# Kernel tuning notes

Hardware: AMD Instinct MI355X
Metric: run time of the kernel (lower is better)

Reference implementation:

```python
import jax, jax.numpy as jnp
import numpy as np

N_NODES = 50000
N_FEATURES = 128
HIDDEN = 64
N_EDGES = 1600000


def gcn_conv(x, src, dst, edge_w, W, b, num_nodes):
    """torch_geometric GCNConv with edge weights: add self-loops (weight 1),
    symmetric deg^-1/2 normalization, aggregate into dst, then bias."""
    loop = jnp.arange(num_nodes)
    src_f = jnp.concatenate([src, loop])
    dst_f = jnp.concatenate([dst, loop])
    w_f = jnp.concatenate([edge_w, jnp.ones((num_nodes,), dtype=edge_w.dtype)])
    deg = jax.ops.segment_sum(w_f, dst_f, num_segments=num_nodes)
    dinv = jnp.where(deg > 0, jax.lax.rsqrt(deg), 0.0)
    norm = dinv[src_f] * w_f * dinv[dst_f]            # [E+N]
    h = x @ W                                          # [N, out]
    msg = h[src_f] * norm[:, None]                     # [E+N, out]
    out = jax.ops.segment_sum(msg, dst_f, num_segments=num_nodes)
    return out + b


def setup_inputs() -> dict:
    key = jax.random.key(0)
    ks = jax.random.split(key, 12)
    features = jax.random.normal(ks[0], (N_NODES, N_FEATURES), dtype=jnp.float32)
    edge_index = jax.random.randint(ks[1], (2, N_EDGES), 0, N_NODES, dtype=jnp.int64)
    edge_attr = jax.random.uniform(ks[2], (N_EDGES,), dtype=jnp.float32)
    s = 0.05
    W1 = jax.random.normal(ks[3], (N_FEATURES, HIDDEN), dtype=jnp.float32) * s
    b1 = jnp.zeros((HIDDEN,), dtype=jnp.float32)
    W2 = jax.random.normal(ks[4], (HIDDEN, HIDDEN // 2), dtype=jnp.float32) * s
    b2 = jnp.zeros((HIDDEN // 2,), dtype=jnp.float32)
    Wd = jax.random.normal(ks[5], (N_FEATURES, 2), dtype=jnp.float32) * s
    bd = jnp.zeros((2,), dtype=jnp.float32)
    w_fc = jax.random.normal(ks[6], (N_NODES * 2,), dtype=jnp.float32) * s
    b_fc = jnp.zeros((), dtype=jnp.float32)
    return {"features": features, "edge_index": edge_index, "edge_attr": edge_attr,
            "W1": W1, "b1": b1, "W2": W2, "b2": b2, "Wd": Wd, "bd": bd,
            "w_fc": w_fc, "b_fc": b_fc}


def reference(features, edge_index, edge_attr, W1, b1, W2, b2, Wd, bd, w_fc, b_fc):
    N = features.shape[0]
    src, dst = edge_index[0], edge_index[1]
    # --- generator encoder (GAE.encode): GCN -> relu -> GCN -> tanh ---
    h = gcn_conv(features, src, dst, edge_attr, W1, b1, N)
    h = jax.nn.relu(h)                                  # dropout inactive (eval)
    z = jnp.tanh(gcn_conv(h, src, dst, edge_attr, W2, b2, N))  # [N, HIDDEN//2]
    # --- residual path: tile z to n_features width and add input features ---
    rep = features.shape[1] // z.shape[1]
    x = jnp.tile(z, (1, rep)) + features                # [N, n_features]
    # (edge_probabilities = z@z.T + rebuilt adjacency is computed by the
    #  generator but discarded by GraphCounteRGAN.forward -> dead code)
    # --- discriminator: GCN -> relu -> flatten -> fc -> sigmoid ---
    d = jax.nn.relu(gcn_conv(x, src, dst, edge_attr, Wd, bd, N))  # [N, 2]
    logit = jnp.dot(d.reshape(-1), w_fc) + b_fc
    return jax.nn.sigmoid(logit)
```

## Files before the change

kernel.cpp:

```cpp
#include <hip/hip_runtime.h>
#include <math.h>

#define BLK 256
#define CHUNK 4096
#define BSH 8
#define BNODES 256
#define MAXNB 256

typedef __attribute__((ext_vector_type(8))) short bf8_t;
typedef __attribute__((ext_vector_type(4))) float f4_t;

__device__ __forceinline__ unsigned short f2bf(float f) {
    unsigned u = __float_as_uint(f);
    u += 0x7FFFu + ((u >> 16) & 1u);
    return (unsigned short)(u >> 16);
}
__device__ __forceinline__ float bf2f(unsigned short b) {
    return __uint_as_float(((unsigned)b) << 16);
}

__global__ void detect_kernel(const int* __restrict__ idx, int E,
                              int* __restrict__ flag, float* __restrict__ acc,
                              int* __restrict__ done) {
    int t = threadIdx.x;
    long long j = (long long)t * (E / 64);
    int hi = idx[2 * j + 1];
    unsigned long long b = __ballot(hi != 0);
    if (t == 0) { *flag = (b == 0ULL) ? 1 : 0; *acc = 0.f; *done = 0; }
}

__global__ __launch_bounds__(256) void bucket_hist_kernel(const int* __restrict__ idx,
                                                          int* __restrict__ blockCnt,
                                                          int E, int NB) {
    __shared__ int hist[MAXNB];
    __shared__ int i64s;
    int t = threadIdx.x;
    for (int i = t; i < NB; i += 256) hist[i] = 0;
    if (t < 64) {
        long long j = (long long)t * (E / 64);
        int hi = idx[2 * j + 1];
        unsigned long long b = __ballot(hi != 0);
        if (t == 0) i64s = (b == 0ULL) ? 1 : 0;
    }
    __syncthreads();
    bool i64 = i64s != 0;
    int e0 = blockIdx.x * CHUNK;
    int e1 = min(e0 + CHUNK, E);
    for (int e = e0 + t; e < e1; e += 256) {
        int d = i64 ? idx[2 * (E + e)] : idx[E + e];
        atomicAdd(&hist[d >> BSH], 1);
    }
    __syncthreads();
    for (int i = t; i < NB; i += 256) blockCnt[blockIdx.x * NB + i] = hist[i];
}

__global__ __launch_bounds__(256) void col_scan_kernel(const int* __restrict__ blockCnt,
                                                       int* __restrict__ blockBase,
                                                       int* __restrict__ bucketTotal,
                                                       int NBLK, int NB,
                                                       float* __restrict__ acc,
                                                       int* __restrict__ done) {
    __shared__ int s[256];
    __shared__ int carry;
    int bkt = blockIdx.x;
    int t = threadIdx.x;
    if (bkt == 0 && t == 0) { *acc = 0.f; *done = 0; }
    if (t == 0) carry = 0;
    __syncthreads();
    for (int base = 0; base < NBLK; base += 256) {
        int i = base + t;
        int v = (i < NBLK) ? blockCnt[i * NB + bkt] : 0;
        s[t] = v;
        __syncthreads();
        for (int off = 1; off < 256; off <<= 1) {
            int x = (t >= off) ? s[t - off] : 0;
            __syncthreads();
            s[t] += x;
            __syncthreads();
        }
        if (i < NBLK) blockBase[i * NB + bkt] = carry + s[t] - v;
        __syncthreads();
        if (t == 0) carry += s[255];
        __syncthreads();
    }
    if (t == 0) bucketTotal[bkt] = carry;
}

__global__ __launch_bounds__(256) void bucket_scatter_kernel(const int* __restrict__ idx,
                                                             const float* __restrict__ ew,
                                                             const int* __restrict__ bucketTotal,
                                                             const int* __restrict__ blockBase,
                                                             int2* __restrict__ temp,
                                                             int E, int NB) {
    __shared__ int base[MAXNB];
    __shared__ int fill[MAXNB];
    __shared__ int s[256];
    __shared__ int i64s;
    int t = threadIdx.x;
    int v = (t < NB) ? bucketTotal[t] : 0;
    s[t] = v;
    if (t < 64) {
        long long j = (long long)t * (E / 64);
        int hi = idx[2 * j + 1];
        unsigned long long b = __ballot(hi != 0);
        if (t == 0) i64s = (b == 0ULL) ? 1 : 0;
    }
    __syncthreads();
    for (int off = 1; off < 256; off <<= 1) {
        int x = (t >= off) ? s[t - off] : 0;
        __syncthreads();
        s[t] += x;
        __syncthreads();
    }
    if (t < NB) {
        base[t] = (s[t] - v) + blockBase[blockIdx.x * NB + t];
        fill[t] = 0;
    }
    __syncthreads();
    bool i64 = i64s != 0;
    int e0 = blockIdx.x * CHUNK;
    int e1 = min(e0 + CHUNK, E);
    for (int e = e0 + t; e < e1; e += 256) {
        int s_, d;
        if (i64) { s_ = idx[2 * e]; d = idx[2 * (E + e)]; }
        else     { s_ = idx[e];     d = idx[E + e]; }
        float w = ew[e];
        int b = d >> BSH;
        int pos = base[b] + atomicAdd(&fill[b], 1);
        temp[pos] = make_int2(s_ | ((d & (BNODES - 1)) << 16), __float_as_int(w));
    }
}

__global__ __launch_bounds__(512) void csr_build_kernel(const int2* __restrict__ temp,
                                                        const int* __restrict__ bucketTotal,
                                                        unsigned* __restrict__ csrw,
                                                        int* __restrict__ row,
                                                        float* __restrict__ dinv,
                                                        int N, int NB, int E) {
    __shared__ int cnt[BNODES];
    __shared__ float dw[BNODES];
    __shared__ int offs[BNODES];
    __shared__ int sb[256];
    int bkt = blockIdx.x;
    int t = threadIdx.x;
    int node0 = bkt << BSH;
    int nn = min(BNODES, N - node0);
    if (t < BNODES) { cnt[t] = 0; dw[t] = 0.f; }
    if (t < 256) sb[t] = (t < NB) ? bucketTotal[t] : 0;
    __syncthreads();
    for (int off = 1; off < 256; off <<= 1) {
        int x = 0;
        if (t < 256 && t >= off) x = sb[t - off];
        __syncthreads();
        if (t < 256) sb[t] += x;
        __syncthreads();
    }
    int p0 = (bkt > 0) ? sb[bkt - 1] : 0;
    int p1 = sb[bkt];
    for (int p = p0 + t; p < p1; p += 512) {
        int2 v = temp[p];
        int dl = (v.x >> 16) & (BNODES - 1);
        atomicAdd(&cnt[dl], 1);
        atomicAdd(&dw[dl], __int_as_float(v.y));
    }
    __syncthreads();
    int v = 0;
    if (t < BNODES) { v = cnt[t]; offs[t] = v; }
    __syncthreads();
    for (int off = 1; off < BNODES; off <<= 1) {
        int x = 0;
        if (t < BNODES && t >= off) x = offs[t - off];
        __syncthreads();
        if (t < BNODES) offs[t] += x;
        __syncthreads();
    }
    if (t < BNODES) {
        int excl = offs[t] - v;
        if (t < nn) {
            row[node0 + t] = p0 + excl;
            dinv[node0 + t] = rsqrtf(1.f + dw[t]);
        }
        offs[t] = excl;
    }
    if (bkt == NB - 1 && t == 0) row[N] = E;
    __syncthreads();
    if (t < BNODES) cnt[t] = 0;
    __syncthreads();
    for (int p = p0 + t; p < p1; p += 512) {
        int2 v2 = temp[p];
        int dl = (v2.x >> 16) & (BNODES - 1);
        int pos = p0 + offs[dl] + atomicAdd(&cnt[dl], 1);
        unsigned wb = (unsigned)v2.y;
        wb += 0x7FFFu + ((wb >> 16) & 1u);
        csrw[pos] = ((unsigned)v2.x & 0xFFFFu) | (wb & 0xFFFF0000u);
    }
}

__global__ __launch_bounds__(256) void gather64_kernel(const int* __restrict__ row,
                                                       const unsigned* __restrict__ csrw,
                                                       const unsigned short* __restrict__ h,
                                                       const float* __restrict__ dinv,
                                                       const float* __restrict__ bias,
                                                       float* __restrict__ out, int N) {
    int wid = (blockIdx.x * 256 + threadIdx.x) >> 6;
    int o = threadIdx.x & 63;
    if (wid >= N) return;
    float di = dinv[wid];
    int p0 = row[wid], p1 = row[wid + 1];
    const unsigned short* hb = h + o;
    float es[4] = {0.f, 0.f, 0.f, 0.f};
    for (int p = p0; p < p1; p += 64) {
        int q = p + o;
        unsigned pe = (q < p1) ? csrw[q] : 0u;
        int m = min(64, p1 - p);
        int mp = (m + 15) & ~15;
        for (int j = 0; j < mp; j += 16) {
            unsigned ee[16];
            float hh[16];
#pragma unroll
            for (int u = 0; u < 16; ++u) ee[u] = (unsigned)__shfl((int)pe, j + u, 64);
#pragma unroll
            for (int u = 0; u < 16; ++u) hh[u] = bf2f(hb[(ee[u] & 0xFFFFu) * 64]);
#pragma unroll
            for (int u = 0; u < 16; ++u)
                es[u & 3] = fmaf(__uint_as_float(ee[u] & 0xFFFF0000u), hh[u], es[u & 3]);
        }
    }
    float e01 = es[0] + es[1], e23 = es[2] + es[3];
    out[wid * 64 + o] = bias[o] + di * (bf2f(h[(size_t)wid * 64 + o]) + e01 + e23);
}

__global__ __launch_bounds__(256) void gather32_kernel(const int* __restrict__ row,
                                                       const unsigned* __restrict__ csrw,
                                                       const unsigned short* __restrict__ h,
                                                       const float* __restrict__ dinv,
                                                       const float* __restrict__ bias,
                                                       float* __restrict__ out, int N) {
    int wid = (blockIdx.x * 256 + threadIdx.x) >> 6;
    int lane = threadIdx.x & 63;
    int o = lane & 31;
    int g = lane >> 5;
    if (wid >= N) return;
    float di = dinv[wid];
    int p0 = row[wid], p1 = row[wid + 1];
    const unsigned short* hb = h + o;
    float es[4] = {0.f, 0.f, 0.f, 0.f};
    for (int p = p0; p < p1; p += 64) {
        int q = p + lane;
        unsigned pe = (q < p1) ? csrw[q] : 0u;
        int m = min(64, p1 - p);
        int mp = (m + 15) & ~15;
        for (int j = g; j < mp; j += 16) {
            unsigned ee[8];
            float hh[8];
#pragma unroll
            for (int u = 0; u < 8; ++u) ee[u] = (unsigned)__shfl((int)pe, j + 2 * u, 64);
#pragma unroll
            for (int u = 0; u < 8; ++u) hh[u] = bf2f(hb[(ee[u] & 0xFFFFu) * 32]);
#pragma unroll
            for (int u = 0; u < 8; ++u)
                es[u & 3] = fmaf(__uint_as_float(ee[u] & 0xFFFF0000u), hh[u], es[u & 3]);
        }
    }
    float es_t = (es[0] + es[1]) + (es[2] + es[3]);
    es_t += __shfl_down(es_t, 32, 64);
    if (g == 0) out[wid * 32 + o] = bias[o] + di * (bf2f(h[wid * 32 + o]) + es_t);
}

__global__ __launch_bounds__(256) void gather2_kernel(const int* __restrict__ row,
                                                      const unsigned* __restrict__ csrw,
                                                      const unsigned short* __restrict__ h,
                                                      const float* __restrict__ dinv,
                                                      const float* __restrict__ bias,
                                                      float* __restrict__ out, int N) {
    const unsigned* hp = (const unsigned*)h;
    int wid = (blockIdx.x * 256 + threadIdx.x) >> 6;
    int lane = threadIdx.x & 63;
    if (wid >= N) return;
    float di = dinv[wid];
    int p0 = row[wid], p1 = row[wid + 1];
    float a0 = 0.f, a1 = 0.f, b0 = 0.f, b1 = 0.f;
    int p = p0 + lane;
    for (; p + 64 < p1; p += 128) {
        unsigned pe0 = csrw[p];
        unsigned pe1 = csrw[p + 64];
        unsigned hw0 = hp[pe0 & 0xFFFFu];
        unsigned hw1 = hp[pe1 & 0xFFFFu];
        float w0 = __uint_as_float(pe0 & 0xFFFF0000u);
        float w1 = __uint_as_float(pe1 & 0xFFFF0000u);
        a0 = fmaf(w0, __uint_as_float(hw0 << 16), a0);
        a1 = fmaf(w0, __uint_as_float(hw0 & 0xFFFF0000u), a1);
        b0 = fmaf(w1, __uint_as_float(hw1 << 16), b0);
        b1 = fmaf(w1, __uint_as_float(hw1 & 0xFFFF0000u), b1);
    }
    if (p < p1) {
        unsigned pe0 = csrw[p];
        unsigned hw0 = hp[pe0 & 0xFFFFu];
        float w0 = __uint_as_float(pe0 & 0xFFFF0000u);
        a0 = fmaf(w0, __uint_as_float(hw0 << 16), a0);
        a1 = fmaf(w0, __uint_as_float(hw0 & 0xFFFF0000u), a1);
    }
    a0 += b0; a1 += b1;
#pragma unroll
    for (int off = 32; off > 0; off >>= 1) {
        a0 += __shfl_down(a0, off, 64);
        a1 += __shfl_down(a1, off, 64);
    }
    if (lane == 0) {
        unsigned hw = hp[wid];
        out[wid * 2 + 0] = bias[0] + di * (__uint_as_float(hw << 16) + a0);
        out[wid * 2 + 1] = bias[1] + di * (__uint_as_float(hw & 0xFFFF0000u) + a1);
    }
}

__global__ __launch_bounds__(256) void mm1_mfma_kernel(const float* __restrict__ X,
                                                       const float* __restrict__ W,
                                                       const float* __restrict__ dinv,
                                                       unsigned short* __restrict__ Y, int N) {
    __shared__ unsigned short Wf[4 * 4 * 64 * 8];
    int t = threadIdx.x;
    for (int i = t; i < 8192; i += 256) {
        int j = i & 7;
        int lane = (i >> 3) & 63;
        int ct = (i >> 9) & 3;
        int kt = i >> 11;
        int k = kt * 32 + (lane >> 4) * 8 + j;
        int c = ct * 16 + (lane & 15);
        Wf[i] = f2bf(W[k * 64 + c]);
    }
    __syncthreads();
    int wave = t >> 6, lane = t & 63;
    int row0 = blockIdx.x * 64 + wave * 16;
    if (row0 >= N) return;
    int r = row0 + (lane & 15);
    int kq = (lane >> 4) * 8;
    bool rv = r < N;
    f4_t acc0 = {0.f, 0.f, 0.f, 0.f}, acc1 = acc0, acc2 = acc0, acc3 = acc0;
    const bf8_t* wf = (const bf8_t*)Wf;
#pragma unroll
    for (int kt = 0; kt < 4; ++kt) {
        bf8_t a = {0, 0, 0, 0, 0, 0, 0, 0};
        if (rv) {
            const float4* ap = (const float4*)(X + (size_t)r * 128 + kt * 32 + kq);
            float4 lo = ap[0], hi = ap[1];
            a[0] = (short)f2bf(lo.x); a[1] = (short)f2bf(lo.y);
            a[2] = (short)f2bf(lo.z); a[3] = (short)f2bf(lo.w);
            a[4] = (short)f2bf(hi.x); a[5] = (short)f2bf(hi.y);
            a[6] = (short)f2bf(hi.z); a[7] = (short)f2bf(hi.w);
        }
        bf8_t b0 = wf[(kt * 4 + 0) * 64 + lane];
        bf8_t b1 = wf[(kt * 4 + 1) * 64 + lane];
        bf8_t b2 = wf[(kt * 4 + 2) * 64 + lane];
        bf8_t b3 = wf[(kt * 4 + 3) * 64 + lane];
        acc0 = __builtin_amdgcn_mfma_f32_16x16x32_bf16(a, b0, acc0, 0, 0, 0);
        acc1 = __builtin_amdgcn_mfma_f32_16x16x32_bf16(a, b1, acc1, 0, 0, 0);
        acc2 = __builtin_amdgcn_mfma_f32_16x16x32_bf16(a, b2, acc2, 0, 0, 0);
        acc3 = __builtin_amdgcn_mfma_f32_16x16x32_bf16(a, b3, acc3, 0, 0, 0);
    }
    int colb = lane & 15;
    int rbase = row0 + (lane >> 4) * 4;
#pragma unroll
    for (int reg = 0; reg < 4; ++reg) {
        int rr = rbase + reg;
        if (rr < N) {
            float dv = dinv[rr];
            Y[(size_t)rr * 64 + colb]      = f2bf(dv * acc0[reg]);
            Y[(size_t)rr * 64 + 16 + colb] = f2bf(dv * acc1[reg]);
            Y[(size_t)rr * 64 + 32 + colb] = f2bf(dv * acc2[reg]);
            Y[(size_t)rr * 64 + 48 + colb] = f2bf(dv * acc3[reg]);
        }
    }
}

__global__ __launch_bounds__(256) void mm2_mfma_kernel(const float* __restrict__ A,
                                                       const float* __restrict__ W,
                                                       const float* __restrict__ dinv,
                                                       unsigned short* __restrict__ Y, int N) {
    __shared__ unsigned short Wf[2 * 2 * 64 * 8];
    int t = threadIdx.x;
    for (int i = t; i < 2048; i += 256) {
        int j = i & 7;
        int lane = (i >> 3) & 63;
        int ct = (i >> 9) & 1;
        int kt = i >> 10;
        int k = kt * 32 + (lane >> 4) * 8 + j;
        int c = ct * 16 + (lane & 15);
        Wf[i] = f2bf(W[k * 32 + c]);
    }
    __syncthreads();
    int wave = t >> 6, lane = t & 63;
    int row0 = blockIdx.x * 64 + wave * 16;
    if (row0 >= N) return;
    int r = row0 + (lane & 15);
    int kq = (lane >> 4) * 8;
    bool rv = r < N;
    f4_t acc0 = {0.f, 0.f, 0.f, 0.f}, acc1 = acc0;
    const bf8_t* wf = (const bf8_t*)Wf;
#pragma unroll
    for (int kt = 0; kt < 2; ++kt) {
        bf8_t a = {0, 0, 0, 0, 0, 0, 0, 0};
        if (rv) {
            const float4* ap = (const float4*)(A + (size_t)r * 64 + kt * 32 + kq);
            float4 lo = ap[0], hi = ap[1];
            a[0] = (short)f2bf(fmaxf(lo.x, 0.f)); a[1] = (short)f2bf(fmaxf(lo.y, 0.f));
            a[2] = (short)f2bf(fmaxf(lo.z, 0.f)); a[3] = (short)f2bf(fmaxf(lo.w, 0.f));
            a[4] = (short)f2bf(fmaxf(hi.x, 0.f)); a[5] = (short)f2bf(fmaxf(hi.y, 0.f));
            a[6] = (short)f2bf(fmaxf(hi.z, 0.f)); a[7] = (short)f2bf(fmaxf(hi.w, 0.f));
        }
        bf8_t b0 = wf[(kt * 2 + 0) * 64 + lane];
        bf8_t b1 = wf[(kt * 2 + 1) * 64 + lane];
        acc0 = __builtin_amdgcn_mfma_f32_16x16x32_bf16(a, b0, acc0, 0, 0, 0);
        acc1 = __builtin_amdgcn_mfma_f32_16x16x32_bf16(a, b1, acc1, 0, 0, 0);
    }
    int colb = lane & 15;
    int rbase = row0 + (lane >> 4) * 4;
#pragma unroll
    for (int reg = 0; reg < 4; ++reg) {
        int rr = rbase + reg;
        if (rr < N) {
            float dv = dinv[rr];
            Y[(size_t)rr * 32 + colb]      = f2bf(dv * acc0[reg]);
            Y[(size_t)rr * 32 + 16 + colb] = f2bf(dv * acc1[reg]);
        }
    }
}

__global__ __launch_bounds__(256) void disc_mm_kernel(const float* __restrict__ Z,
                                                      const float* __restrict__ F,
                                                      const float* __restrict__ Wd,
                                                      const float* __restrict__ dinv,
                                                      unsigned short* __restrict__ Y, int N) {
    __shared__ float Ws[256];
    if (threadIdx.x < 256) Ws[threadIdx.x] = Wd[threadIdx.x];
    __syncthreads();
    int n = blockIdx.x * 256 + threadIdx.x;
    if (n >= N) return;
    float zt[32];
#pragma unroll
    for (int j = 0; j < 32; ++j) zt[j] = tanhf(Z[n * 32 + j]);
    float a0 = 0.f, a1 = 0.f;
    const float* fr = F + (size_t)n * 128;
#pragma unroll 4
    for (int c = 0; c < 128; ++c) {
        float xv = zt[c & 31] + fr[c];
        a0 = fmaf(xv, Ws[c * 2 + 0], a0);
        a1 = fmaf(xv, Ws[c * 2 + 1], a1);
    }
    float dv = dinv[n];
    ushort2 o;
    o.x = f2bf(dv * a0); o.y = f2bf(dv * a1);
    ((ushort2*)Y)[n] = o;
}

__global__ void init_deg_kernel(float* __restrict__ deg, int N) {
    int n = blockIdx.x * BLK + threadIdx.x;
    if (n < N) deg[n] = 1.0f;
}

__global__ void edge_deg_kernel(const int* __restrict__ idx, const float* __restrict__ ew,
                                const int* __restrict__ flag, float* __restrict__ deg, int E) {
    int e = blockIdx.x * BLK + threadIdx.x;
    if (e >= E) return;
    int d = (*flag) ? idx[2 * (E + e)] : idx[E + e];
    atomicAdd(&deg[d], ew[e]);
}

__global__ void dinv_kernel(float* __restrict__ deg, int N) {
    int n = blockIdx.x * BLK + threadIdx.x;
    if (n < N) deg[n] = rsqrtf(deg[n]);
}

template <int WD>
__global__ void init_agg_kernel(const unsigned short* __restrict__ h, const float* __restrict__ dinv,
                                const float* __restrict__ bias, float* __restrict__ agg, int N) {
    int i = blockIdx.x * BLK + threadIdx.x;
    if (i >= N * WD) return;
    int n = i / WD, o = i % WD;
    float di = dinv[n];
    agg[i] = bias[o] + di * bf2f(h[i]);
}

template <int WD>
__global__ void edge_agg_kernel(const int* __restrict__ idx, const float* __restrict__ ew,
                                const int* __restrict__ flag, const float* __restrict__ dinv,
                                const unsigned short* __restrict__ h, float* __restrict__ agg, int E) {
    int gid = blockIdx.x * BLK + threadIdx.x;
    if (gid >= E * WD) return;
    int e = gid / WD;
    int o = gid % WD;
    int s, d;
    if (*flag) { s = idx[2 * e]; d = idx[2 * (E + e)]; }
    else       { s = idx[e];     d = idx[E + e]; }
    float nrm = ew[e] * dinv[d];
    atomicAdd(&agg[d * WD + o], nrm * bf2f(h[s * WD + o]));
}

__global__ void reduce_final_kernel(const float* __restrict__ dmat, const float* __restrict__ wfc,
                                    float* __restrict__ acc, int* __restrict__ done,
                                    const float* __restrict__ bfc, float* __restrict__ out,
                                    int M, int nblk) {
    int i = blockIdx.x * BLK + threadIdx.x;
    float v = 0.f;
    if (i < M) v = fmaxf(dmat[i], 0.f) * wfc[i];
#pragma unroll
    for (int off = 32; off > 0; off >>= 1) v += __shfl_down(v, off, 64);
    if ((threadIdx.x & 63) == 0) atomicAdd(acc, v);
    __syncthreads();
    if (threadIdx.x == 0) {
        __threadfence();
        int old = atomicAdd(done, 1);
        if (old == nblk - 1) {
            float x = atomicAdd(acc, 0.f) + *bfc;
            out[0] = 1.f / (1.f + expf(-x));
        }
    }
}

extern "C" void kernel_launch(void* const* d_in, const int* in_sizes, int n_in,
                              void* d_out, int out_size, void* d_ws, size_t ws_size,
                              hipStream_t stream) {
    const float* feat = (const float*)d_in[0];
    const int*   eidx = (const int*)d_in[1];
    const float* ew   = (const float*)d_in[2];
    const float* W1   = (const float*)d_in[3];
    const float* b1   = (const float*)d_in[4];
    const float* W2   = (const float*)d_in[5];
    const float* b2   = (const float*)d_in[6];
    const float* Wd   = (const float*)d_in[7];
    const float* bd   = (const float*)d_in[8];
    const float* wfc  = (const float*)d_in[9];
    const float* bfc  = (const float*)d_in[10];

    const int N = in_sizes[0] / 128;
    const int E = in_sizes[2];

    const int NB   = (N + BNODES - 1) >> BSH;
    const int NBLK = (E + CHUNK - 1) / CHUNK;

    float* ws = (float*)d_ws;
    size_t u = 0;
    float* dinv = ws + u; u += N;
    if (u & 1) u++;
    size_t M1 = ((size_t)N * 32 > (size_t)E * 2) ? (size_t)N * 32 : (size_t)E * 2;
    unsigned short* h = (unsigned short*)(ws + u); int2* temp = (int2*)h; u += M1;
    if (u & 1) u++;
    float* agg = ws + u; u += (size_t)N * 64;
    float* acc = ws + u; u += 1;
    int* flag = (int*)(ws + u); u += 1;
    int* done = (int*)(ws + u); u += 1;
    int* row  = (int*)(ws + u); u += (size_t)N + 1;
    int* bucketTotal = (int*)(ws + u); u += NB;
    int* blockCnt    = (int*)(ws + u); u += (size_t)NBLK * NB;
    int* blockBase   = (int*)(ws + u); u += (size_t)NBLK * NB;
    unsigned* csrw   = (unsigned*)(ws + u); u += (size_t)E;
    size_t need = u * 4;

    float* out = (float*)d_out;

    const int gN = (N + BLK - 1) / BLK;
    const int gE = (E + BLK - 1) / BLK;
    const int gW = (N + 3) / 4;
    const int gM = (N + 63) / 64;
    const int gR = (N * 2 + BLK - 1) / BLK;

    if (ws_size >= need && N <= 65536 && NB <= MAXNB) {
        hipLaunchKernelGGL(bucket_hist_kernel, dim3(NBLK), dim3(256), 0, stream,
                           eidx, blockCnt, E, NB);
        hipLaunchKernelGGL(col_scan_kernel, dim3(NB), dim3(256), 0, stream,
                           blockCnt, blockBase, bucketTotal, NBLK, NB, acc, done);
        hipLaunchKernelGGL(bucket_scatter_kernel, dim3(NBLK), dim3(256), 0, stream,
                           eidx, ew, bucketTotal, blockBase, temp, E, NB);
        hipLaunchKernelGGL(csr_build_kernel, dim3(NB), dim3(512), 0, stream,
                           temp, bucketTotal, csrw, row, dinv, N, NB, E);

        hipLaunchKernelGGL(mm1_mfma_kernel, dim3(gM), dim3(256), 0, stream,
                           feat, W1, dinv, h, N);
        hipLaunchKernelGGL(gather64_kernel, dim3(gW), dim3(256), 0, stream,
                           row, csrw, h, dinv, b1, agg, N);
        hipLaunchKernelGGL(mm2_mfma_kernel, dim3(gM), dim3(256), 0, stream,
                           agg, W2, dinv, h, N);
        hipLaunchKernelGGL(gather32_kernel, dim3(gW), dim3(256), 0, stream,
                           row, csrw, h, dinv, b2, agg, N);
        hipLaunchKernelGGL(disc_mm_kernel, dim3((N + 255) / 256), dim3(256), 0, stream,
                           agg, feat, Wd, dinv, h, N);
        hipLaunchKernelGGL(gather2_kernel, dim3(gW), dim3(256), 0, stream,
                           row, csrw, h, dinv, bd, agg, N);
    } else {
        hipLaunchKernelGGL(detect_kernel, dim3(1), dim3(64), 0, stream, eidx, E, flag, acc, done);
        hipLaunchKernelGGL(init_deg_kernel, dim3(gN), dim3(BLK), 0, stream, dinv, N);
        hipLaunchKernelGGL(edge_deg_kernel, dim3(gE), dim3(BLK), 0, stream, eidx, ew, flag, dinv, E);
        hipLaunchKernelGGL(dinv_kernel, dim3(gN), dim3(BLK), 0, stream, dinv, N);

        hipLaunchKernelGGL(mm1_mfma_kernel, dim3(gM), dim3(256), 0, stream, feat, W1, dinv, h, N);
        hipLaunchKernelGGL((init_agg_kernel<64>), dim3((N * 64 + BLK - 1) / BLK), dim3(BLK), 0, stream,
                           h, dinv, b1, agg, N);
        hipLaunchKernelGGL((edge_agg_kernel<64>), dim3((E / BLK) * 64 + 64), dim3(BLK), 0, stream,
                           eidx, ew, flag, dinv, h, agg, E);
        hipLaunchKernelGGL(mm2_mfma_kernel, dim3(gM), dim3(256), 0, stream, agg, W2, dinv, h, N);
        hipLaunchKernelGGL((init_agg_kernel<32>), dim3((N * 32 + BLK - 1) / BLK), dim3(BLK), 0, stream,
                           h, dinv, b2, agg, N);
        hipLaunchKernelGGL((edge_agg_kernel<32>), dim3((E / BLK) * 32 + 32), dim3(BLK), 0, stream,
                           eidx, ew, flag, dinv, h, agg, E);
        hipLaunchKernelGGL(disc_mm_kernel, dim3((N + 255) / 256), dim3(256), 0, stream,
                           agg, feat, Wd, dinv, h, N);
        hipLaunchKernelGGL((init_agg_kernel<2>), dim3((N * 2 + BLK - 1) / BLK), dim3(BLK), 0, stream,
                           h, dinv, bd, agg, N);
        hipLaunchKernelGGL((edge_agg_kernel<2>), dim3((E * 2 + BLK - 1) / BLK), dim3(BLK), 0, stream,
                           eidx, ew, flag, dinv, h, agg, E);
    }

    hipLaunchKernelGGL(reduce_final_kernel, dim3(gR), dim3(BLK), 0, stream,
                       agg, wfc, acc, done, bfc, out, N * 2, gR);
}
```

Measured before the change: 272.1 us.

## Replace column scan with atomic bucket offsets and fuse disc matmul and final reduction

The per-block bucket histogram now claims its base offset with a global atomicAdd, which removes the separate column-scan kernel and the blockCnt buffer. CHUNK is doubled to halve the number of bucketing blocks. The tanh, residual add and discriminator matmul are fused into the layer-2 gather kernel, and the layer-3 gather is fused with the relu, fc dot product and sigmoid reduction. Together this cuts three kernel launches and the intermediate global traffic between them. In exchange, edge order within each bucket now depends on atomic timing, so results are nondeterministic, and a memset is added to the stream.

```diff
diff --git a/kernel.cpp b/kernel.cpp
--- a/kernel.cpp
+++ b/kernel.cpp
@@ -2,7 +2,7 @@
 #include <math.h>
 
 #define BLK 256
-#define CHUNK 4096
+#define CHUNK 8192
 #define BSH 8
 #define BNODES 256
 #define MAXNB 256
@@ -30,7 +30,8 @@
 }
 
 __global__ __launch_bounds__(256) void bucket_hist_kernel(const int* __restrict__ idx,
-                                                          int* __restrict__ blockCnt,
+                                                          int* __restrict__ bucketFill,
+                                                          int* __restrict__ blockBase,
                                                           int E, int NB) {
     __shared__ int hist[MAXNB];
     __shared__ int i64s;
@@ -51,44 +52,13 @@
         atomicAdd(&hist[d >> BSH], 1);
     }
     __syncthreads();
-    for (int i = t; i < NB; i += 256) blockCnt[blockIdx.x * NB + i] = hist[i];
-}
-
-__global__ __launch_bounds__(256) void col_scan_kernel(const int* __restrict__ blockCnt,
-                                                       int* __restrict__ blockBase,
-                                                       int* __restrict__ bucketTotal,
-                                                       int NBLK, int NB,
-                                                       float* __restrict__ acc,
-                                                       int* __restrict__ done) {
-    __shared__ int s[256];
-    __shared__ int carry;
-    int bkt = blockIdx.x;
-    int t = threadIdx.x;
-    if (bkt == 0 && t == 0) { *acc = 0.f; *done = 0; }
-    if (t == 0) carry = 0;
-    __syncthreads();
-    for (int base = 0; base < NBLK; base += 256) {
-        int i = base + t;
-        int v = (i < NBLK) ? blockCnt[i * NB + bkt] : 0;
-        s[t] = v;
-        __syncthreads();
-        for (int off = 1; off < 256; off <<= 1) {
-            int x = (t >= off) ? s[t - off] : 0;
-            __syncthreads();
-            s[t] += x;
-            __syncthreads();
-        }
-        if (i < NBLK) blockBase[i * NB + bkt] = carry + s[t] - v;
-        __syncthreads();
-        if (t == 0) carry += s[255];
-        __syncthreads();
-    }
-    if (t == 0) bucketTotal[bkt] = carry;
+    for (int i = t; i < NB; i += 256)
+        blockBase[blockIdx.x * NB + i] = atomicAdd(&bucketFill[i], hist[i]);
 }
 
 __global__ __launch_bounds__(256) void bucket_scatter_kernel(const int* __restrict__ idx,
                                                              const float* __restrict__ ew,
-                                                             const int* __restrict__ bucketTotal,
+                                                             const int* __restrict__ bucketFill,
                                                              const int* __restrict__ blockBase,
                                                              int2* __restrict__ temp,
                                                              int E, int NB) {
@@ -97,7 +67,7 @@
     __shared__ int s[256];
     __shared__ int i64s;
     int t = threadIdx.x;
-    int v = (t < NB) ? bucketTotal[t] : 0;
+    int v = (t < NB) ? bucketFill[t] : 0;
     s[t] = v;
     if (t < 64) {
         long long j = (long long)t * (E / 64);
@@ -132,7 +102,7 @@
 }
 
 __global__ __launch_bounds__(512) void csr_build_kernel(const int2* __restrict__ temp,
-                                                        const int* __restrict__ bucketTotal,
+                                                        const int* __restrict__ bucketFill,
                                                         unsigned* __restrict__ csrw,
                                                         int* __restrict__ row,
                                                         float* __restrict__ dinv,
@@ -146,7 +116,7 @@
     int node0 = bkt << BSH;
     int nn = min(BNODES, N - node0);
     if (t < BNODES) { cnt[t] = 0; dw[t] = 0.f; }
-    if (t < 256) sb[t] = (t < NB) ? bucketTotal[t] : 0;
+    if (t < 256) sb[t] = (t < NB) ? bucketFill[t] : 0;
     __syncthreads();
     for (int off = 1; off < 256; off <<= 1) {
         int x = 0;
@@ -230,12 +200,18 @@
     out[wid * 64 + o] = bias[o] + di * (bf2f(h[(size_t)wid * 64 + o]) + e01 + e23);
 }
 
-__global__ __launch_bounds__(256) void gather32_kernel(const int* __restrict__ row,
-                                                       const unsigned* __restrict__ csrw,
-                                                       const unsigned short* __restrict__ h,
-                                                       const float* __restrict__ dinv,
-                                                       const float* __restrict__ bias,
-                                                       float* __restrict__ out, int N) {
+__global__ __launch_bounds__(256) void gather32_disc_kernel(const int* __restrict__ row,
+                                                            const unsigned* __restrict__ csrw,
+                                                            const unsigned short* __restrict__ h,
+                                                            const float* __restrict__ dinv,
+                                                            const float* __restrict__ bias,
+                                                            const float* __restrict__ F,
+                                                            const float* __restrict__ Wd,
+                                                            unsigned short* __restrict__ hout,
+                                                            int N) {
+    __shared__ float Ws[256];
+    if (threadIdx.x < 256) Ws[threadIdx.x] = Wd[threadIdx.x];
+    __syncthreads();
     int wid = (blockIdx.x * 256 + threadIdx.x) >> 6;
     int lane = threadIdx.x & 63;
     int o = lane & 31;
@@ -264,52 +240,95 @@
     }
     float es_t = (es[0] + es[1]) + (es[2] + es[3]);
     es_t += __shfl_down(es_t, 32, 64);
-    if (g == 0) out[wid * 32 + o] = bias[o] + di * (bf2f(h[wid * 32 + o]) + es_t);
-}
-
-__global__ __launch_bounds__(256) void gather2_kernel(const int* __restrict__ row,
-                                                      const unsigned* __restrict__ csrw,
-                                                      const unsigned short* __restrict__ h,
-                                                      const float* __restrict__ dinv,
-                                                      const float* __restrict__ bias,
-                                                      float* __restrict__ out, int N) {
+    float a0 = 0.f, a1 = 0.f;
+    if (g == 0) {
+        float zt = tanhf(bias[o] + di * (bf2f(h[wid * 32 + o]) + es_t));
+        const float* fr = F + (size_t)wid * 128;
+#pragma unroll
+        for (int j = 0; j < 4; ++j) {
+            int c = o + 32 * j;
+            float xv = zt + fr[c];
+            a0 = fmaf(xv, Ws[c * 2 + 0], a0);
+            a1 = fmaf(xv, Ws[c * 2 + 1], a1);
+        }
+    }
+#pragma unroll
+    for (int off = 16; off > 0; off >>= 1) {
+        a0 += __shfl_down(a0, off, 64);
+        a1 += __shfl_down(a1, off, 64);
+    }
+    if (lane == 0) {
+        ushort2 ov;
+        ov.x = f2bf(di * a0);
+        ov.y = f2bf(di * a1);
+        ((ushort2*)hout)[wid] = ov;
+    }
+}
+
+__global__ __launch_bounds__(256) void gather2_reduce_kernel(const int* __restrict__ row,
+                                                             const unsigned* __restrict__ csrw,
+                                                             const unsigned short* __restrict__ h,
+                                                             const float* __restrict__ dinv,
+                                                             const float* __restrict__ bias,
+                                                             const float* __restrict__ wfc,
+                                                             float* __restrict__ acc,
+                                                             int* __restrict__ done,
+                                                             const float* __restrict__ bfc,
+                                                             float* __restrict__ out,
+                                                             int N, int nblk) {
     const unsigned* hp = (const unsigned*)h;
+    __shared__ float wsum[4];
     int wid = (blockIdx.x * 256 + threadIdx.x) >> 6;
     int lane = threadIdx.x & 63;
-    if (wid >= N) return;
-    float di = dinv[wid];
-    int p0 = row[wid], p1 = row[wid + 1];
-    float a0 = 0.f, a1 = 0.f, b0 = 0.f, b1 = 0.f;
-    int p = p0 + lane;
-    for (; p + 64 < p1; p += 128) {
-        unsigned pe0 = csrw[p];
-        unsigned pe1 = csrw[p + 64];
-        unsigned hw0 = hp[pe0 & 0xFFFFu];
-        unsigned hw1 = hp[pe1 & 0xFFFFu];
-        float w0 = __uint_as_float(pe0 & 0xFFFF0000u);
-        float w1 = __uint_as_float(pe1 & 0xFFFF0000u);
-        a0 = fmaf(w0, __uint_as_float(hw0 << 16), a0);
-        a1 = fmaf(w0, __uint_as_float(hw0 & 0xFFFF0000u), a1);
-        b0 = fmaf(w1, __uint_as_float(hw1 << 16), b0);
-        b1 = fmaf(w1, __uint_as_float(hw1 & 0xFFFF0000u), b1);
-    }
-    if (p < p1) {
-        unsigned pe0 = csrw[p];
-        unsigned hw0 = hp[pe0 & 0xFFFFu];
-        float w0 = __uint_as_float(pe0 & 0xFFFF0000u);
-        a0 = fmaf(w0, __uint_as_float(hw0 << 16), a0);
-        a1 = fmaf(w0, __uint_as_float(hw0 & 0xFFFF0000u), a1);
-    }
-    a0 += b0; a1 += b1;
-#pragma unroll
-    for (int off = 32; off > 0; off >>= 1) {
-        a0 += __shfl_down(a0, off, 64);
-        a1 += __shfl_down(a1, off, 64);
-    }
-    if (lane == 0) {
-        unsigned hw = hp[wid];
-        out[wid * 2 + 0] = bias[0] + di * (__uint_as_float(hw << 16) + a0);
-        out[wid * 2 + 1] = bias[1] + di * (__uint_as_float(hw & 0xFFFF0000u) + a1);
+    float contrib = 0.f;
+    if (wid < N) {
+        float di = dinv[wid];
+        int p0 = row[wid], p1 = row[wid + 1];
+        float a0 = 0.f, a1 = 0.f, b0 = 0.f, b1 = 0.f;
+        int p = p0 + lane;
+        for (; p + 64 < p1; p += 128) {
+            unsigned pe0 = csrw[p];
+            unsigned pe1 = csrw[p + 64];
+            unsigned hw0 = hp[pe0 & 0xFFFFu];
+            unsigned hw1 = hp[pe1 & 0xFFFFu];
+            float w0 = __uint_as_float(pe0 & 0xFFFF0000u);
+            float w1 = __uint_as_float(pe1 & 0xFFFF0000u);
+            a0 = fmaf(w0, __uint_as_float(hw0 << 16), a0);
+            a1 = fmaf(w0, __uint_as_float(hw0 & 0xFFFF0000u), a1);
+            b0 = fmaf(w1, __uint_as_float(hw1 << 16), b0);
+            b1 = fmaf(w1, __uint_as_float(hw1 & 0xFFFF0000u), b1);
+        }
+        if (p < p1) {
+            unsigned pe0 = csrw[p];
+            unsigned hw0 = hp[pe0 & 0xFFFFu];
+            float w0 = __uint_as_float(pe0 & 0xFFFF0000u);
+            a0 = fmaf(w0, __uint_as_float(hw0 << 16), a0);
+            a1 = fmaf(w0, __uint_as_float(hw0 & 0xFFFF0000u), a1);
+        }
+        a0 += b0; a1 += b1;
+#pragma unroll
+        for (int off = 32; off > 0; off >>= 1) {
+            a0 += __shfl_down(a0, off, 64);
+            a1 += __shfl_down(a1, off, 64);
+        }
+        if (lane == 0) {
+            unsigned hw = hp[wid];
+            float v0 = bias[0] + di * (__uint_as_float(hw << 16) + a0);
+            float v1 = bias[1] + di * (__uint_as_float(hw & 0xFFFF0000u) + a1);
+            contrib = fmaxf(v0, 0.f) * wfc[wid * 2 + 0] + fmaxf(v1, 0.f) * wfc[wid * 2 + 1];
+        }
+    }
+    if ((threadIdx.x & 63) == 0) wsum[threadIdx.x >> 6] = contrib;
+    __syncthreads();
+    if (threadIdx.x == 0) {
+        float s = (wsum[0] + wsum[1]) + (wsum[2] + wsum[3]);
+        atomicAdd(acc, s);
+        __threadfence();
+        int old = atomicAdd(done, 1);
+        if (old == nblk - 1) {
+            float x = atomicAdd(acc, 0.f) + *bfc;
+            out[0] = 1.f / (1.f + expf(-x));
+        }
     }
 }
 
@@ -545,14 +564,13 @@
     unsigned short* h = (unsigned short*)(ws + u); int2* temp = (int2*)h; u += M1;
     if (u & 1) u++;
     float* agg = ws + u; u += (size_t)N * 64;
+    int* bucketFill = (int*)(ws + u); u += NB;
     float* acc = ws + u; u += 1;
+    int* done = (int*)(ws + u); u += 1;
     int* flag = (int*)(ws + u); u += 1;
-    int* done = (int*)(ws + u); u += 1;
     int* row  = (int*)(ws + u); u += (size_t)N + 1;
-    int* bucketTotal = (int*)(ws + u); u += NB;
-    int* blockCnt    = (int*)(ws + u); u += (size_t)NBLK * NB;
-    int* blockBase   = (int*)(ws + u); u += (size_t)NBLK * NB;
-    unsigned* csrw   = (unsigned*)(ws + u); u += (size_t)E;
+    int* blockBase = (int*)(ws + u); u += (size_t)NBLK * NB;
+    unsigned* csrw = (unsigned*)(ws + u); u += (size_t)E;
     size_t need = u * 4;
 
     float* out = (float*)d_out;
@@ -564,14 +582,13 @@
     const int gR = (N * 2 + BLK - 1) / BLK;
 
     if (ws_size >= need && N <= 65536 && NB <= MAXNB) {
+        hipMemsetAsync(bucketFill, 0, (size_t)(NB + 2) * 4, stream);
         hipLaunchKernelGGL(bucket_hist_kernel, dim3(NBLK), dim3(256), 0, stream,
-                           eidx, blockCnt, E, NB);
-        hipLaunchKernelGGL(col_scan_kernel, dim3(NB), dim3(256), 0, stream,
-                           blockCnt, blockBase, bucketTotal, NBLK, NB, acc, done);
+                           eidx, bucketFill, blockBase, E, NB);
         hipLaunchKernelGGL(bucket_scatter_kernel, dim3(NBLK), dim3(256), 0, stream,
-                           eidx, ew, bucketTotal, blockBase, temp, E, NB);
+                           eidx, ew, bucketFill, blockBase, temp, E, NB);
         hipLaunchKernelGGL(csr_build_kernel, dim3(NB), dim3(512), 0, stream,
-                           temp, bucketTotal, csrw, row, dinv, N, NB, E);
+                           temp, bucketFill, csrw, row, dinv, N, NB, E);
 
         hipLaunchKernelGGL(mm1_mfma_kernel, dim3(gM), dim3(256), 0, stream,
                            feat, W1, dinv, h, N);
@@ -579,12 +596,11 @@
                            row, csrw, h, dinv, b1, agg, N);
         hipLaunchKernelGGL(mm2_mfma_kernel, dim3(gM), dim3(256), 0, stream,
                            agg, W2, dinv, h, N);
-        hipLaunchKernelGGL(gather32_kernel, dim3(gW), dim3(256), 0, stream,
-                           row, csrw, h, dinv, b2, agg, N);
-        hipLaunchKernelGGL(disc_mm_kernel, dim3((N + 255) / 256), dim3(256), 0, stream,
-                           agg, feat, Wd, dinv, h, N);
-        hipLaunchKernelGGL(gather2_kernel, dim3(gW), dim3(256), 0, stream,
-                           row, csrw, h, dinv, bd, agg, N);
+        hipLaunchKernelGGL(gather32_disc_kernel, dim3(gW), dim3(256), 0, stream,
+                           row, csrw, h, dinv, b2, feat, Wd, (unsigned short*)agg, N);
+        hipLaunchKernelGGL(gather2_reduce_kernel, dim3(gW), dim3(256), 0, stream,
+                           row, csrw, (const unsigned short*)agg, dinv, bd, wfc,
+                           acc, done, bfc, out, N, gW);
     } else {
         hipLaunchKernelGGL(detect_kernel, dim3(1), dim3(64), 0, stream, eidx, E, flag, acc, done);
         hipLaunchKernelGGL(init_deg_kernel, dim3(gN), dim3(BLK), 0, stream, dinv, N);
@@ -607,8 +623,7 @@
                            h, dinv, bd, agg, N);
         hipLaunchKernelGGL((edge_agg_kernel<2>), dim3((E * 2 + BLK - 1) / BLK), dim3(BLK), 0, stream,
                            eidx, ew, flag, dinv, h, agg, E);
-    }
-
-    hipLaunchKernelGGL(reduce_final_kernel, dim3(gR), dim3(BLK), 0, stream,
-                       agg, wfc, acc, done, bfc, out, N * 2, gR);
-}
+        hipLaunchKernelGGL(reduce_final_kernel, dim3(gR), dim3(BLK), 0, stream,
+                           agg, wfc, acc, done, bfc, out, N * 2, gR);
+    }
+}
```

After: 545.9 us. 2.01x slower.
